# Optimization experiments

Measured on AMD Instinct MI355X. Metric: run time of the kernel, lower is better.

## Reference

```python
import jax, jax.numpy as jnp
import numpy as np

B, NUM_SLOTS, D, TOP_K = 2048, 128, 1024, 8
DH = D // 2  # route_mlp hidden


def setup_inputs() -> dict:
    key = jax.random.key(0)
    ks = jax.random.split(key, 16)
    s = 0.02
    return {
        "x": jax.random.normal(ks[0], (B, D), jnp.float32),
        "S": jax.random.normal(ks[1], (B, NUM_SLOTS, D), jnp.float32),
        # route_mlp: Linear(2D, D//2) -> GELU -> Linear(D//2, NUM_SLOTS)
        "w1": jax.random.normal(ks[2], (DH, 2 * D), jnp.float32) * s,
        "b1": jnp.zeros((DH,), jnp.float32),
        "w2": jax.random.normal(ks[3], (NUM_SLOTS, DH), jnp.float32) * s,
        "b2": jnp.zeros((NUM_SLOTS,), jnp.float32),
        # GRUCell(D, D): torch layout, gates ordered (r, z, n)
        "gru_wih": jax.random.normal(ks[4], (3 * D, D), jnp.float32) * s,
        "gru_whh": jax.random.normal(ks[5], (3 * D, D), jnp.float32) * s,
        "gru_bih": jnp.zeros((3 * D,), jnp.float32),
        "gru_bhh": jnp.zeros((3 * D,), jnp.float32),
        "wval": jax.random.normal(ks[6], (D, D), jnp.float32) * s,
        "bval": jnp.zeros((D,), jnp.float32),
        "wout": jax.random.normal(ks[7], (D, D), jnp.float32) * s,
        "bout": jnp.zeros((D,), jnp.float32),
        "tau": jnp.ones((1,), jnp.float32),
    }


def reference(x, S, w1, b1, w2, b2, gru_wih, gru_whh, gru_bih, gru_bhh,
              wval, bval, wout, bout, tau):
    # Routing: context = [x, mean over slots]
    slot_mean = S.mean(axis=1)                                  # [B, D]
    ctx = jnp.concatenate([x, slot_mean], axis=-1)              # [B, 2D]
    h = jax.nn.gelu(ctx @ w1.T + b1, approximate=False)         # [B, DH]
    route_logits = (h @ w2.T + b2) / (jnp.abs(tau) + 0.1)       # [B, NUM_SLOTS]

    topk_vals, topk_idx = jax.lax.top_k(route_logits, TOP_K)    # [B, K]
    topk_w = jax.nn.softmax(topk_vals, axis=-1)                 # [B, K]

    # Gather selected slot states
    slot_states = jnp.take_along_axis(S, topk_idx[:, :, None], axis=1)  # [B, K, D]

    # GRUCell (torch semantics). Input part shared across the K slots.
    gi = x @ gru_wih.T + gru_bih                                # [B, 3D]
    gh = slot_states @ gru_whh.T + gru_bhh                      # [B, K, 3D]
    gi_r, gi_z, gi_n = jnp.split(gi, 3, axis=-1)
    gh_r, gh_z, gh_n = jnp.split(gh, 3, axis=-1)
    r = jax.nn.sigmoid(gi_r[:, None, :] + gh_r)
    z = jax.nn.sigmoid(gi_z[:, None, :] + gh_z)
    n = jnp.tanh(gi_n[:, None, :] + r * gh_n)
    updated = (1.0 - z) * n + z * slot_states                   # [B, K, D]

    # Scatter updated states back into slot memory
    S_new = S.at[jnp.arange(B)[:, None], topk_idx].set(updated)

    # Weighted value readout
    values = updated @ wval.T + bval                            # [B, K, D]
    mixed = jnp.einsum('bkd,bk->bd', values, topk_w)            # [B, D]
    output = mixed @ wout.T + bout                              # [B, D]
    return output, S_new
```

## Files before the change

### kernel.cpp

```cpp
#include <hip/hip_runtime.h>
#include <math.h>
#include <stdint.h>

#define B_   2048
#define NS_  128
#define D_   1024
#define K_   8
#define DH_  512
#define G3_  3072

typedef unsigned short u16;
typedef short bf16x8 __attribute__((ext_vector_type(8)));
typedef float f32x4 __attribute__((ext_vector_type(4)));

__device__ __forceinline__ float bf2f(u16 u) {
  union { unsigned i; float f; } v; v.i = ((unsigned)u) << 16; return v.f;
}
__device__ __forceinline__ u16 f2bf(float f) {
  unsigned x = __float_as_uint(f);
  return (u16)((x + 0x7fffu + ((x >> 16) & 1u)) >> 16);
}

#define AS1C(p) ((const __attribute__((address_space(1))) void*)(uintptr_t)(p))
#define AS3(p)  ((__attribute__((address_space(3))) void*)(unsigned)(uintptr_t)(p))

template<int DO_COPY>
__global__ __launch_bounds__(256)
void sp_copymean(const float* __restrict__ S, float* __restrict__ Snew,
                 float* __restrict__ mean) {
  const int b = blockIdx.x;
  const int t = threadIdx.x, d0 = t * 4;
  const f32x4* src = (const f32x4*)(S + (size_t)b * NS_ * D_) + t;
  f32x4* dst = (f32x4*)(Snew + (size_t)b * NS_ * D_) + t;
  double a0 = 0, a1 = 0, a2 = 0, a3 = 0;
  #pragma unroll 4
  for (int s = 0; s < NS_; ++s) {
    f32x4 v = __builtin_nontemporal_load(src);
    if (DO_COPY) __builtin_nontemporal_store(v, dst);
    a0 += v[0]; a1 += v[1]; a2 += v[2]; a3 += v[3];
    src += 256; dst += 256;
  }
  float4 m;
  m.x = (float)(a0 * (1.0 / 128.0)); m.y = (float)(a1 * (1.0 / 128.0));
  m.z = (float)(a2 * (1.0 / 128.0)); m.w = (float)(a3 * (1.0 / 128.0));
  *(float4*)&mean[(size_t)b * D_ + d0] = m;
}

__global__ __launch_bounds__(256)
void sp_convert_all(const float* __restrict__ x, const float* __restrict__ wih,
                    const float* __restrict__ whh, const float* __restrict__ wval,
                    const float* __restrict__ wout,
                    u16* __restrict__ xb, u16* __restrict__ wihb,
                    u16* __restrict__ whhb, u16* __restrict__ wvalb,
                    u16* __restrict__ woutb) {
  const int stride = gridDim.x * 256;
  for (int i = blockIdx.x * 256 + threadIdx.x; i < 2621440; i += stride) {
    const float* s; u16* d; int off;
    if (i < 524288)       { s = x;    d = xb;    off = i; }
    else if (i < 1310720) { s = wih;  d = wihb;  off = i - 524288; }
    else if (i < 2097152) { s = whh;  d = whhb;  off = i - 1310720; }
    else if (i < 2359296) { s = wval; d = wvalb; off = i - 2097152; }
    else                  { s = wout; d = woutb; off = i - 2359296; }
    float4 v = ((const float4*)s)[off];
    ushort4 o;
    o.x = f2bf(v.x); o.y = f2bf(v.y); o.z = f2bf(v.z); o.w = f2bf(v.w);
    ((ushort4*)d)[off] = o;
  }
}

__global__ __launch_bounds__(256)
void sp_gemm1(const float* __restrict__ x, const float* __restrict__ mean,
              const float* __restrict__ w1, const float* __restrict__ bias1,
              float* __restrict__ h) {
  __shared__ float As[16][68];
  __shared__ float Bs[16][36];
  int wg = blockIdx.x;
  wg = (wg & 7) * 64 + (wg >> 3);
  const int n0 = (wg & 15) * 32;
  const int m0 = (wg >> 4) * 64;
  const int t = threadIdx.x;
  const int tx = t & 15, ty = t >> 4;
  float acc[4][2] = {};
  const int sr = t >> 2, sc = (t & 3) * 4;
  for (int k0 = 0; k0 < 2 * D_; k0 += 16) {
    const float* src = (k0 < D_) ? (x + k0) : (mean + (k0 - D_));
    float4 va = *(const float4*)&src[(size_t)(m0 + sr) * D_ + sc];
    As[sc + 0][sr] = va.x; As[sc + 1][sr] = va.y; As[sc + 2][sr] = va.z; As[sc + 3][sr] = va.w;
    if (t < 128) {
      const int bn = t >> 2, bc = (t & 3) * 4;
      float4 vb = *(const float4*)&w1[(size_t)(n0 + bn) * (2 * D_) + k0 + bc];
      Bs[bc + 0][bn] = vb.x; Bs[bc + 1][bn] = vb.y; Bs[bc + 2][bn] = vb.z; Bs[bc + 3][bn] = vb.w;
    }
    __syncthreads();
    #pragma unroll
    for (int kk = 0; kk < 16; ++kk) {
      float4 a = *(const float4*)&As[kk][ty * 4];
      float2 bb = *(const float2*)&Bs[kk][tx * 2];
      acc[0][0] = fmaf(a.x, bb.x, acc[0][0]); acc[0][1] = fmaf(a.x, bb.y, acc[0][1]);
      acc[1][0] = fmaf(a.y, bb.x, acc[1][0]); acc[1][1] = fmaf(a.y, bb.y, acc[1][1]);
      acc[2][0] = fmaf(a.z, bb.x, acc[2][0]); acc[2][1] = fmaf(a.z, bb.y, acc[2][1]);
      acc[3][0] = fmaf(a.w, bb.x, acc[3][0]); acc[3][1] = fmaf(a.w, bb.y, acc[3][1]);
    }
    __syncthreads();
  }
  #pragma unroll
  for (int i = 0; i < 4; ++i) {
    #pragma unroll
    for (int j = 0; j < 2; ++j) {
      const int r = m0 + ty * 4 + i, c = n0 + tx * 2 + j;
      float v = acc[i][j] + bias1[c];
      v = 0.5f * v * (1.0f + erff(v * 0.70710678118654752f));
      h[(size_t)r * DH_ + c] = v;
    }
  }
}

__global__ __launch_bounds__(64)
void sp_route_topk(const float* __restrict__ h, const float* __restrict__ w2,
                   const float* __restrict__ b2, const float* __restrict__ tau,
                   int* __restrict__ tki, float* __restrict__ tkw) {
  __shared__ float hs[DH_];
  const int b = blockIdx.x, l = threadIdx.x;
  *(float4*)&hs[l * 4] = *(const float4*)&h[(size_t)b * DH_ + l * 4];
  *(float4*)&hs[256 + l * 4] = *(const float4*)&h[(size_t)b * DH_ + 256 + l * 4];
  __syncthreads();
  const double invd = 1.0 / ((double)fabsf(tau[0]) + 0.1);
  float v[2]; int id[2];
  #pragma unroll
  for (int c = 0; c < 2; ++c) {
    const int n = c * 64 + l;
    const float* wr = &w2[(size_t)n * DH_];
    double s = 0.0;
    for (int j = 0; j < DH_; j += 4) {
      float4 w4 = *(const float4*)&wr[j];
      s += (double)hs[j] * (double)w4.x;
      s += (double)hs[j + 1] * (double)w4.y;
      s += (double)hs[j + 2] * (double)w4.z;
      s += (double)hs[j + 3] * (double)w4.w;
    }
    v[c] = (float)((s + (double)b2[n]) * invd);
    id[c] = n;
  }
  float m0f = 0.f, sum = 0.f, mye = 0.f; int myi = 0;
  for (int r = 0; r < 8; ++r) {
    float mv; int mi;
    if (v[1] > v[0]) { mv = v[1]; mi = id[1]; } else { mv = v[0]; mi = id[0]; }
    #pragma unroll
    for (int off = 32; off > 0; off >>= 1) {
      float ov = __shfl_xor(mv, off);
      int oi = __shfl_xor(mi, off);
      if (ov > mv || (ov == mv && oi < mi)) { mv = ov; mi = oi; }
    }
    if (r == 0) m0f = mv;
    float er = expf(mv - m0f);
    sum += er;
    if (l == r) { mye = er; myi = mi; }
    if (mi == id[0]) v[0] = -3.0e38f;
    if (mi == id[1]) v[1] = -3.0e38f;
  }
  if (l < 8) { tki[b * K_ + l] = myi; tkw[b * K_ + l] = mye / sum; }
}

__global__ __launch_bounds__(256)
void sp_gather(const float* __restrict__ S, const int* __restrict__ tki,
               u16* __restrict__ slotb) {
  const int blk = blockIdx.x;
  const int b = blk >> 3, k = blk & 7;
  const int s = tki[b * K_ + k];
  const int t = threadIdx.x;
  float4 v = *(const float4*)&S[((size_t)b * NS_ + s) * D_ + t * 4];
  ushort4 o;
  o.x = f2bf(v.x); o.y = f2bf(v.y); o.z = f2bf(v.z); o.w = f2bf(v.w);
  *(ushort4*)&slotb[((size_t)b * K_ + k) * D_ + t * 4] = o;
}

template<int EPI>
__global__ __launch_bounds__(256)
void sp_gemm_bf16(const u16* __restrict__ A, const u16* __restrict__ Bm,
                  void* __restrict__ Cv, const float* __restrict__ bias,
                  int M, int N, int Kd, int nbx) {
  __shared__ u16 lA[128 * 32];
  __shared__ u16 lB[128 * 32];
  int wg = blockIdx.x;
  {
    const int nwg = nbx * ((M + 127) >> 7);
    const int cpx = nwg >> 3;
    wg = (wg & 7) * cpx + (wg >> 3);
  }
  const int m0 = (wg / nbx) * 128, n0 = (wg % nbx) * 128;
  const int t = threadIdx.x;
  const int lane = t & 63;
  const int w = t >> 6;
  const int wm = w >> 1, wn = w & 1;

  f32x4 acc[4][4] = {};

  const int srow = t >> 2;
  const int scol = (t & 3) * 8;
  const u16* gA0 = A + (size_t)(m0 + srow) * Kd + scol;
  const u16* gA1 = A + (size_t)(m0 + 64 + srow) * Kd + scol;
  const u16* gB0 = Bm + (size_t)(n0 + srow) * Kd + scol;
  const u16* gB1 = Bm + (size_t)(n0 + 64 + srow) * Kd + scol;
  u16* lAw = &lA[(t & 192) * 8];
  u16* lBw = &lB[(t & 192) * 8];

  const int kb = (lane >> 4) * 8;
  const int rA = wm * 64 + (lane & 15);
  const int rB = wn * 64 + (lane & 15);

  for (int k0 = 0; k0 < Kd; k0 += 32) {
    __builtin_amdgcn_global_load_lds(AS1C(gA0 + k0), AS3(lAw), 16, 0, 0);
    __builtin_amdgcn_global_load_lds(AS1C(gA1 + k0), AS3(lAw + 2048), 16, 0, 0);
    __builtin_amdgcn_global_load_lds(AS1C(gB0 + k0), AS3(lBw), 16, 0, 0);
    __builtin_amdgcn_global_load_lds(AS1C(gB1 + k0), AS3(lBw + 2048), 16, 0, 0);
    __syncthreads();
    bf16x8 af[4], bfr[4];
    #pragma unroll
    for (int fm = 0; fm < 4; ++fm)
      af[fm] = *(const bf16x8*)&lA[(rA + fm * 16) * 32 + kb];
    #pragma unroll
    for (int fn = 0; fn < 4; ++fn)
      bfr[fn] = *(const bf16x8*)&lB[(rB + fn * 16) * 32 + kb];
    #pragma unroll
    for (int fm = 0; fm < 4; ++fm) {
      #pragma unroll
      for (int fn = 0; fn < 4; ++fn)
        acc[fm][fn] = __builtin_amdgcn_mfma_f32_16x16x32_bf16(af[fm], bfr[fn], acc[fm][fn], 0, 0, 0);
    }
    __syncthreads();
  }

  #pragma unroll
  for (int fm = 0; fm < 4; ++fm) {
    #pragma unroll
    for (int fn = 0; fn < 4; ++fn) {
      #pragma unroll
      for (int i = 0; i < 4; ++i) {
        const int r = m0 + wm * 64 + fm * 16 + (lane >> 4) * 4 + i;
        const int c = n0 + wn * 64 + fn * 16 + (lane & 15);
        float v = acc[fm][fn][i];
        if constexpr (EPI >= 2) v += bias[c];
        if constexpr (EPI == 0 || EPI == 2)
          ((float*)Cv)[(size_t)r * N + c] = v;
        else
          ((u16*)Cv)[(size_t)r * N + c] = f2bf(v);
      }
    }
  }
}

template<bool DIRECT>
__global__ __launch_bounds__(256)
void sp_gru(const float* __restrict__ gi, const u16* __restrict__ gh,
            const float* __restrict__ S, const int* __restrict__ tki,
            const float* __restrict__ tkw, const float* __restrict__ bih,
            const float* __restrict__ bhh, float* __restrict__ dst,
            u16* __restrict__ umix) {
  const int b = blockIdx.x, t = threadIdx.x;
  const int d0 = t * 4;
  float Gr[4], Gz[4], Gn[4], Hr[4], Hz[4], Hn[4], Um[4] = {0.f, 0.f, 0.f, 0.f};
  {
    const size_t gb = (size_t)b * G3_;
    float4 a, c;
    a = *(const float4*)&gi[gb + d0];          c = *(const float4*)&bih[d0];
    Gr[0]=a.x+c.x; Gr[1]=a.y+c.y; Gr[2]=a.z+c.z; Gr[3]=a.w+c.w;
    a = *(const float4*)&gi[gb + D_ + d0];     c = *(const float4*)&bih[D_ + d0];
    Gz[0]=a.x+c.x; Gz[1]=a.y+c.y; Gz[2]=a.z+c.z; Gz[3]=a.w+c.w;
    a = *(const float4*)&gi[gb + 2 * D_ + d0]; c = *(const float4*)&bih[2 * D_ + d0];
    Gn[0]=a.x+c.x; Gn[1]=a.y+c.y; Gn[2]=a.z+c.z; Gn[3]=a.w+c.w;
    c = *(const float4*)&bhh[d0];          Hr[0]=c.x; Hr[1]=c.y; Hr[2]=c.z; Hr[3]=c.w;
    c = *(const float4*)&bhh[D_ + d0];     Hz[0]=c.x; Hz[1]=c.y; Hz[2]=c.z; Hz[3]=c.w;
    c = *(const float4*)&bhh[2 * D_ + d0]; Hn[0]=c.x; Hn[1]=c.y; Hn[2]=c.z; Hn[3]=c.w;
  }
  #pragma unroll
  for (int k = 0; k < K_; ++k) {
    const int s = tki[b * K_ + k];
    const float wk = tkw[b * K_ + k];
    const float4 sl = *(const float4*)&S[((size_t)b * NS_ + s) * D_ + d0];
    const u16* ghp = gh + ((size_t)b * K_ + k) * G3_ + d0;
    ushort4 r4 = *(const ushort4*)(ghp);
    ushort4 z4 = *(const ushort4*)(ghp + D_);
    ushort4 n4 = *(const ushort4*)(ghp + 2 * D_);
    float slc[4] = { sl.x, sl.y, sl.z, sl.w };
    u16 rr[4] = { r4.x, r4.y, r4.z, r4.w };
    u16 zz[4] = { z4.x, z4.y, z4.z, z4.w };
    u16 nn[4] = { n4.x, n4.y, n4.z, n4.w };
    float uv[4];
    #pragma unroll
    for (int j = 0; j < 4; ++j) {
      float rg = 1.f / (1.f + expf(-(Gr[j] + bf2f(rr[j]) + Hr[j])));
      float zg = 1.f / (1.f + expf(-(Gz[j] + bf2f(zz[j]) + Hz[j])));
      float ng = tanhf(Gn[j] + rg * (bf2f(nn[j]) + Hn[j]));
      uv[j] = (1.f - zg) * ng + zg * slc[j];
      Um[j] += wk * uv[j];
    }
    float4 o; o.x = uv[0]; o.y = uv[1]; o.z = uv[2]; o.w = uv[3];
    if (DIRECT)
      *(float4*)&dst[((size_t)b * NS_ + s) * D_ + d0] = o;
    else
      *(float4*)&dst[((size_t)b * K_ + k) * D_ + d0] = o;
  }
  ushort4 um;
  um.x = f2bf(Um[0]); um.y = f2bf(Um[1]); um.z = f2bf(Um[2]); um.w = f2bf(Um[3]);
  *(ushort4*)&umix[(size_t)b * D_ + d0] = um;
}

__global__ __launch_bounds__(256)
void sp_copy_scatter(const float* __restrict__ S, const float* __restrict__ upd,
                     const int* __restrict__ tki, float* __restrict__ Snew) {
  const int b = blockIdx.x, t = threadIdx.x;
  const int d0 = t * 4;
  int idx[K_];
  #pragma unroll
  for (int k = 0; k < K_; ++k) idx[k] = tki[b * K_ + k];
  for (int s = 0; s < NS_; ++s) {
    int sk = -1;
    #pragma unroll
    for (int k = 0; k < K_; ++k) if (idx[k] == s) sk = k;
    float4 v;
    if (sk >= 0) v = *(const float4*)&upd[((size_t)b * K_ + sk) * D_ + d0];
    else         v = *(const float4*)&S[((size_t)b * NS_ + s) * D_ + d0];
    *(float4*)&Snew[((size_t)b * NS_ + s) * D_ + d0] = v;
  }
}

extern "C" void kernel_launch(void* const* d_in, const int* in_sizes, int n_in,
                              void* d_out, int out_size, void* d_ws, size_t ws_size,
                              hipStream_t stream) {
  const float* x    = (const float*)d_in[0];
  const float* S    = (const float*)d_in[1];
  const float* w1   = (const float*)d_in[2];
  const float* b1   = (const float*)d_in[3];
  const float* w2   = (const float*)d_in[4];
  const float* b2   = (const float*)d_in[5];
  const float* wih  = (const float*)d_in[6];
  const float* whh  = (const float*)d_in[7];
  const float* bih  = (const float*)d_in[8];
  const float* bhh  = (const float*)d_in[9];
  const float* wval = (const float*)d_in[10];
  const float* bval = (const float*)d_in[11];
  const float* wout = (const float*)d_in[12];
  const float* bout = (const float*)d_in[13];
  const float* tau  = (const float*)d_in[14];

  float* out  = (float*)d_out;
  float* Snew = out + (size_t)B_ * D_;

  const bool bigws = ws_size >= (size_t)400 * 1024 * 1024;
  char* bigbase = bigws ? (char*)d_ws : (char*)Snew;
  size_t bo = 0;
  auto balloc = [&](size_t bytes) -> void* {
    void* p = bigbase + bo; bo += (bytes + 255) & ~(size_t)255; return p;
  };

  float* mean  = (float*)balloc((size_t)B_ * D_ * 4);
  float* h     = (float*)balloc((size_t)B_ * DH_ * 4);
  u16* xb      = (u16*)balloc((size_t)B_ * D_ * 2);
  u16* wihb    = (u16*)balloc((size_t)G3_ * D_ * 2);
  u16* whhb    = (u16*)balloc((size_t)G3_ * D_ * 2);
  u16* wvalb   = (u16*)balloc((size_t)D_ * D_ * 2);
  u16* woutb   = (u16*)balloc((size_t)D_ * D_ * 2);
  float* gi    = (float*)balloc((size_t)B_ * G3_ * 4);
  u16* slotb   = (u16*)balloc((size_t)B_ * K_ * D_ * 2);
  u16* ghb     = (u16*)balloc((size_t)B_ * K_ * G3_ * 2);
  u16* umixb   = (u16*)balloc((size_t)B_ * D_ * 2);
  u16* mixedb  = (u16*)balloc((size_t)B_ * D_ * 2);

  char* wsb = (char*)d_ws;
  size_t so = bigws ? bo : 0;
  auto salloc = [&](size_t bytes) -> void* {
    void* p = wsb + so; so += (bytes + 255) & ~(size_t)255; return p;
  };
  int*   tki = (int*)salloc((size_t)B_ * K_ * 4);
  float* tkw = (float*)salloc((size_t)B_ * K_ * 4);
  float* upd = bigws ? nullptr : (float*)salloc((size_t)B_ * K_ * D_ * 4);

  if (bigws) sp_copymean<1><<<B_, 256, 0, stream>>>(S, Snew, mean);
  else       sp_copymean<0><<<B_, 256, 0, stream>>>(S, Snew, mean);

  sp_convert_all<<<1024, 256, 0, stream>>>(x, wih, whh, wval, wout,
                                           xb, wihb, whhb, wvalb, woutb);

  sp_gemm1<<<512, 256, 0, stream>>>(x, mean, w1, b1, h);
  sp_route_topk<<<B_, 64, 0, stream>>>(h, w2, b2, tau, tki, tkw);

  sp_gather<<<B_ * K_, 256, 0, stream>>>(S, tki, slotb);

  sp_gemm_bf16<0><<<384, 256, 0, stream>>>(xb, wihb, gi, nullptr, B_, G3_, D_, G3_ / 128);
  sp_gemm_bf16<1><<<3072, 256, 0, stream>>>(slotb, whhb, ghb, nullptr, B_ * K_, G3_, D_, G3_ / 128);

  if (bigws)
    sp_gru<true><<<B_, 256, 0, stream>>>(gi, ghb, S, tki, tkw, bih, bhh, Snew, umixb);
  else
    sp_gru<false><<<B_, 256, 0, stream>>>(gi, ghb, S, tki, tkw, bih, bhh, upd, umixb);

  sp_gemm_bf16<3><<<128, 256, 0, stream>>>(umixb, wvalb, mixedb, bval, B_, D_, D_, D_ / 128);
  sp_gemm_bf16<2><<<128, 256, 0, stream>>>(mixedb, woutb, out, bout, B_, D_, D_, D_ / 128);

  if (!bigws)
    sp_copy_scatter<<<B_, 256, 0, stream>>>(S, upd, tki, Snew);
}
```

Baseline: 897.2 us.

## Fuse hidden-state GRU GEMM with gate epilogue, dropping the gh intermediate

Replaces the separate slot-state x W_hh GEMM and the elementwise GRU kernel with one MFMA kernel. Each block computes a 64-row by 64-column tile for all three gates (r, z, n) and applies the GRU update, scatter write and top-k weighted mix directly from registers. This removes the write and re-read of the large bf16 gh buffer plus one launch. In exchange the GEMM tile is smaller and the K loop is single-buffered with two barriers per step. The slot term in the update now uses the bf16 gathered copy instead of fp32 S, which lowers precision slightly.

```diff
diff --git a/kernel.cpp b/kernel.cpp
--- a/kernel.cpp
+++ b/kernel.cpp
@@ -251,58 +251,101 @@
 
 template<bool DIRECT>
 __global__ __launch_bounds__(256)
-void sp_gru(const float* __restrict__ gi, const u16* __restrict__ gh,
-            const float* __restrict__ S, const int* __restrict__ tki,
-            const float* __restrict__ tkw, const float* __restrict__ bih,
-            const float* __restrict__ bhh, float* __restrict__ dst,
-            u16* __restrict__ umix) {
-  const int b = blockIdx.x, t = threadIdx.x;
-  const int d0 = t * 4;
-  float Gr[4], Gz[4], Gn[4], Hr[4], Hz[4], Hn[4], Um[4] = {0.f, 0.f, 0.f, 0.f};
-  {
-    const size_t gb = (size_t)b * G3_;
-    float4 a, c;
-    a = *(const float4*)&gi[gb + d0];          c = *(const float4*)&bih[d0];
-    Gr[0]=a.x+c.x; Gr[1]=a.y+c.y; Gr[2]=a.z+c.z; Gr[3]=a.w+c.w;
-    a = *(const float4*)&gi[gb + D_ + d0];     c = *(const float4*)&bih[D_ + d0];
-    Gz[0]=a.x+c.x; Gz[1]=a.y+c.y; Gz[2]=a.z+c.z; Gz[3]=a.w+c.w;
-    a = *(const float4*)&gi[gb + 2 * D_ + d0]; c = *(const float4*)&bih[2 * D_ + d0];
-    Gn[0]=a.x+c.x; Gn[1]=a.y+c.y; Gn[2]=a.z+c.z; Gn[3]=a.w+c.w;
-    c = *(const float4*)&bhh[d0];          Hr[0]=c.x; Hr[1]=c.y; Hr[2]=c.z; Hr[3]=c.w;
-    c = *(const float4*)&bhh[D_ + d0];     Hz[0]=c.x; Hz[1]=c.y; Hz[2]=c.z; Hz[3]=c.w;
-    c = *(const float4*)&bhh[2 * D_ + d0]; Hn[0]=c.x; Hn[1]=c.y; Hn[2]=c.z; Hn[3]=c.w;
-  }
+void sp_gh_gru(const u16* __restrict__ slotb, const u16* __restrict__ whhb,
+               const float* __restrict__ gi, const float* __restrict__ bih,
+               const float* __restrict__ bhh, const int* __restrict__ tki,
+               const float* __restrict__ tkw, float* __restrict__ dst,
+               u16* __restrict__ umixb) {
+  __shared__ u16 lA[64 * 32];
+  __shared__ u16 lB[192 * 32];
+  __shared__ int   sTki[64];
+  __shared__ float sTkw[64];
+  int wg = blockIdx.x;
+  wg = (wg & 7) * 512 + (wg >> 3);
+  const int mt = wg >> 4, db = wg & 15;
+  const int m0 = mt * 64, d0 = db * 64;
+  const int t = threadIdx.x;
+  const int lane = t & 63, w = t >> 6;
+  const int wm = w >> 1, wn = w & 1;
+  const int lane15 = lane & 15, hi = lane >> 4;
+
+  if (t < 64) { sTki[t] = tki[m0 + t]; sTkw[t] = tkw[m0 + t]; }
+
+  f32x4 acc[2][6] = {};
+
+  const int srow = t >> 2;
+  const int scol = (t & 3) * 8;
+  const u16* gA  = slotb + (size_t)(m0 + srow) * D_ + scol;
+  const u16* gB0 = whhb + (size_t)(d0 + srow) * D_ + scol;
+  const u16* gB1 = whhb + (size_t)(D_ + d0 + srow) * D_ + scol;
+  const u16* gB2 = whhb + (size_t)(2 * D_ + d0 + srow) * D_ + scol;
+  u16* lAw  = &lA[(t & 192) * 8];
+  u16* lBw0 = &lB[(t & 192) * 8];
+
+  const int kb = hi * 8;
+  const int rA = wm * 32 + lane15;
+  const int rB = wn * 32 + lane15;
+
+  for (int k0 = 0; k0 < D_; k0 += 32) {
+    __builtin_amdgcn_global_load_lds(AS1C(gA  + k0), AS3(lAw), 16, 0, 0);
+    __builtin_amdgcn_global_load_lds(AS1C(gB0 + k0), AS3(lBw0), 16, 0, 0);
+    __builtin_amdgcn_global_load_lds(AS1C(gB1 + k0), AS3(lBw0 + 2048), 16, 0, 0);
+    __builtin_amdgcn_global_load_lds(AS1C(gB2 + k0), AS3(lBw0 + 4096), 16, 0, 0);
+    __syncthreads();
+    bf16x8 af[2], bfr[6];
+    #pragma unroll
+    for (int fm = 0; fm < 2; ++fm)
+      af[fm] = *(const bf16x8*)&lA[(rA + fm * 16) * 32 + kb];
+    #pragma unroll
+    for (int g = 0; g < 3; ++g) {
+      #pragma unroll
+      for (int f = 0; f < 2; ++f)
+        bfr[g * 2 + f] = *(const bf16x8*)&lB[(g * 64 + rB + f * 16) * 32 + kb];
+    }
+    #pragma unroll
+    for (int fm = 0; fm < 2; ++fm) {
+      #pragma unroll
+      for (int fn = 0; fn < 6; ++fn)
+        acc[fm][fn] = __builtin_amdgcn_mfma_f32_16x16x32_bf16(af[fm], bfr[fn], acc[fm][fn], 0, 0, 0);
+    }
+    __syncthreads();
+  }
+
   #pragma unroll
-  for (int k = 0; k < K_; ++k) {
-    const int s = tki[b * K_ + k];
-    const float wk = tkw[b * K_ + k];
-    const float4 sl = *(const float4*)&S[((size_t)b * NS_ + s) * D_ + d0];
-    const u16* ghp = gh + ((size_t)b * K_ + k) * G3_ + d0;
-    ushort4 r4 = *(const ushort4*)(ghp);
-    ushort4 z4 = *(const ushort4*)(ghp + D_);
-    ushort4 n4 = *(const ushort4*)(ghp + 2 * D_);
-    float slc[4] = { sl.x, sl.y, sl.z, sl.w };
-    u16 rr[4] = { r4.x, r4.y, r4.z, r4.w };
-    u16 zz[4] = { z4.x, z4.y, z4.z, z4.w };
-    u16 nn[4] = { n4.x, n4.y, n4.z, n4.w };
-    float uv[4];
-    #pragma unroll
-    for (int j = 0; j < 4; ++j) {
-      float rg = 1.f / (1.f + expf(-(Gr[j] + bf2f(rr[j]) + Hr[j])));
-      float zg = 1.f / (1.f + expf(-(Gz[j] + bf2f(zz[j]) + Hz[j])));
-      float ng = tanhf(Gn[j] + rg * (bf2f(nn[j]) + Hn[j]));
-      uv[j] = (1.f - zg) * ng + zg * slc[j];
-      Um[j] += wk * uv[j];
-    }
-    float4 o; o.x = uv[0]; o.y = uv[1]; o.z = uv[2]; o.w = uv[3];
-    if (DIRECT)
-      *(float4*)&dst[((size_t)b * NS_ + s) * D_ + d0] = o;
-    else
-      *(float4*)&dst[((size_t)b * K_ + k) * D_ + d0] = o;
-  }
-  ushort4 um;
-  um.x = f2bf(Um[0]); um.y = f2bf(Um[1]); um.z = f2bf(Um[2]); um.w = f2bf(Um[3]);
-  *(ushort4*)&umix[(size_t)b * D_ + d0] = um;
+  for (int fm = 0; fm < 2; ++fm) {
+    const int rbase = wm * 32 + fm * 16 + hi * 4;
+    const int bglob = (m0 + rbase) >> 3;
+    #pragma unroll
+    for (int f = 0; f < 2; ++f) {
+      const int dg = d0 + wn * 32 + f * 16 + lane15;
+      const float Gr = gi[(size_t)bglob * G3_ + dg]           + bih[dg];
+      const float Gz = gi[(size_t)bglob * G3_ + D_ + dg]      + bih[D_ + dg];
+      const float Gn = gi[(size_t)bglob * G3_ + 2 * D_ + dg]  + bih[2 * D_ + dg];
+      const float Br = bhh[dg], Bz = bhh[D_ + dg], Bn = bhh[2 * D_ + dg];
+      float part = 0.f;
+      #pragma unroll
+      for (int i = 0; i < 4; ++i) {
+        const int row = rbase + i;
+        const int grow = m0 + row;
+        const float slot = bf2f(slotb[(size_t)grow * D_ + dg]);
+        const float rr = acc[fm][f][i] + Br;
+        const float zz = acc[fm][f + 2][i] + Bz;
+        const float nn = acc[fm][f + 4][i] + Bn;
+        const float rg = 1.f / (1.f + expf(-(Gr + rr)));
+        const float zg = 1.f / (1.f + expf(-(Gz + zz)));
+        const float ng = tanhf(Gn + rg * nn);
+        const float uv = (1.f - zg) * ng + zg * slot;
+        part = fmaf(sTkw[row], uv, part);
+        if (DIRECT)
+          dst[((size_t)bglob * NS_ + sTki[row]) * D_ + dg] = uv;
+        else
+          dst[(size_t)grow * D_ + dg] = uv;
+      }
+      part += __shfl_xor(part, 16);
+      if ((hi & 1) == 0)
+        umixb[(size_t)bglob * D_ + dg] = f2bf(part);
+    }
+  }
 }
 
 __global__ __launch_bounds__(256)
@@ -362,7 +405,6 @@
   u16* woutb   = (u16*)balloc((size_t)D_ * D_ * 2);
   float* gi    = (float*)balloc((size_t)B_ * G3_ * 4);
   u16* slotb   = (u16*)balloc((size_t)B_ * K_ * D_ * 2);
-  u16* ghb     = (u16*)balloc((size_t)B_ * K_ * G3_ * 2);
   u16* umixb   = (u16*)balloc((size_t)B_ * D_ * 2);
   u16* mixedb  = (u16*)balloc((size_t)B_ * D_ * 2);
 
@@ -387,12 +429,13 @@
   sp_gather<<<B_ * K_, 256, 0, stream>>>(S, tki, slotb);
 
   sp_gemm_bf16<0><<<384, 256, 0, stream>>>(xb, wihb, gi, nullptr, B_, G3_, D_, G3_ / 128);
-  sp_gemm_bf16<1><<<3072, 256, 0, stream>>>(slotb, whhb, ghb, nullptr, B_ * K_, G3_, D_, G3_ / 128);
 
   if (bigws)
-    sp_gru<true><<<B_, 256, 0, stream>>>(gi, ghb, S, tki, tkw, bih, bhh, Snew, umixb);
+    sp_gh_gru<true><<<4096, 256, 0, stream>>>(slotb, whhb, gi, bih, bhh,
+                                              tki, tkw, Snew, umixb);
   else
-    sp_gru<false><<<B_, 256, 0, stream>>>(gi, ghb, S, tki, tkw, bih, bhh, upd, umixb);
+    sp_gh_gru<false><<<4096, 256, 0, stream>>>(slotb, whhb, gi, bih, bhh,
+                                               tki, tkw, upd, umixb);
 
   sp_gemm_bf16<3><<<128, 256, 0, stream>>>(umixb, wvalb, mixedb, bval, B_, D_, D_, D_ / 128);
   sp_gemm_bf16<2><<<128, 256, 0, stream>>>(mixedb, woutb, out, bout, B_, D_, D_, D_ / 128);
```

After: 866.3 us. 1.04x faster.
